# Kernel tuning notes

Hardware: AMD Instinct MI355X
Metric: run time of the kernel (lower is better)

The kernel has to match this reference:

```python
import jax, jax.numpy as jnp
import numpy as np

# dims per module source / chosen globals
B, LB = 4, 28            # new frames, buffered frames; M = B+LB = L = 32
DK, DV = 256, 32         # Dk=256 hardcoded; Dv = 4*len_of_lookup+4 with len_of_lookup=7
HS, WS = 64, 64          # H//8, W//8 with H=W=512
LMAX = 32                # memory cap L
TRAIN_SZ = 1000          # log base train_sz
ALPHA = 0.5              # blend coefficient (original inits 0, which zeroes the branch)
# log(L*h*w + h*w, train_sz) / sqrt(Dk)
SCALE = float(np.log(LMAX * HS * WS + HS * WS) / np.log(TRAIN_SZ) / np.sqrt(DK))


def _xavier(key, fan_in, fan_out):
    lim = np.sqrt(6.0 / (fan_in + fan_out))
    return jax.random.uniform(key, (fan_in, fan_out), jnp.float32, -lim, lim)


def setup_inputs() -> dict:
    key = jax.random.key(0)
    ks = jax.random.split(key, 7)
    return {
        "fc": jax.random.normal(ks[0], (B, DK, HS, WS), jnp.float32),
        "fm": jax.random.normal(ks[1], (B, DV, HS, WS), jnp.float32),
        "key_buffer": jax.random.normal(ks[2], (LB, DK, HS, WS), jnp.float32),
        "value_buffer": jax.random.normal(ks[3], (LB, DV, HS, WS), jnp.float32),
        "Q": _xavier(ks[4], DK, DK),
        "K": _xavier(ks[5], DK, DK),
        "V": _xavier(ks[6], DV, DV),
    }


def reference(fc, fm, key_buffer, value_buffer, Q, K, V):
    # matmul = einsum('ijkl,jm->imkl'): per-pixel channel mixing
    q = jnp.einsum('bdhw,de->behw', fc, Q)                      # [B,Dk,h,w]
    k = jnp.concatenate([jnp.einsum('bdhw,de->behw', fc, K), key_buffer], axis=0)    # [M,Dk,h,w]
    v = jnp.concatenate([jnp.einsum('bdhw,de->behw', fm, V), value_buffer], axis=0)  # [M,Dv,h,w]
    # current_batch (=1) < L, so no slicing of k/v on this step
    scores = SCALE * jnp.einsum('bdhw,mdhw->bmhw', q, k)        # [B,M,h,w]
    attn = jax.nn.softmax(scores, axis=-1)                      # NOTE: softmax over width axis, as in source (dim=-1)
    ctx = jnp.einsum('bmhw,mdhw->bdhw', attn, v)                # [B,Dv,h,w]
    return fm + ALPHA * ctx
```

## Files before the change

kernel.cpp:

```cpp
#include <hip/hip_runtime.h>
#include <hip/hip_bf16.h>
#include <cmath>

#define NB 4
#define NM 32
#define DKc 256
#define DVc 32
#define NP 4096

using bf16x8 = __attribute__((ext_vector_type(8))) short;
using f32x4  = __attribute__((ext_vector_type(4))) float;
using f32x2  = __attribute__((ext_vector_type(2))) float;

__device__ __forceinline__ unsigned short f2bf(float f) {
    union { float f; unsigned u; } x; x.f = f;
    unsigned r = 0x7FFFu + ((x.u >> 16) & 1u);
    return (unsigned short)((x.u + r) >> 16);
}

__global__ __launch_bounds__(256) void k_prep(
    const float* __restrict__ fc, unsigned short* __restrict__ fcT,
    const float* __restrict__ Q, unsigned short* __restrict__ WTq,
    const float* __restrict__ K, unsigned short* __restrict__ WTk,
    const float* __restrict__ fm, const float* __restrict__ V, float* __restrict__ vproj) {
    int x = blockIdx.x;
    int t = threadIdx.x;
    if (x < 1056) {
        __shared__ float tile[64][65];
        const float* s; unsigned short* d; int R, C, r0, c0;
        if (x < 1024) {
            int bb = x >> 8, rest = x & 255;
            R = 256; C = 4096;
            r0 = (rest >> 6) * 64; c0 = (rest & 63) * 64;
            s = fc + (long)bb * 256 * 4096; d = fcT + (long)bb * 256 * 4096;
        } else {
            int i = x - 1024;
            int mat = i >> 4, idx = i & 15;
            R = 256; C = 256;
            r0 = (idx >> 2) * 64; c0 = (idx & 3) * 64;
            s = mat ? K : Q; d = mat ? WTk : WTq;
        }
        #pragma unroll
        for (int j = 0; j < 16; ++j) {
            int i = t + 256 * j;
            int r = i >> 6, c = i & 63;
            tile[r][c] = s[(long)(r0 + r) * C + c0 + c];
        }
        __syncthreads();
        #pragma unroll
        for (int j = 0; j < 8; ++j) {
            int i = t + 256 * j;
            int row = i >> 5;
            int pr = i & 31;
            float f0 = tile[2 * pr][row];
            float f1 = tile[2 * pr + 1][row];
            unsigned pack = (unsigned)f2bf(f0) | ((unsigned)f2bf(f1) << 16);
            reinterpret_cast<unsigned*>(d)[(((long)(c0 + row) * R + r0) >> 1) + pr] = pack;
        }
    } else {
        __shared__ float Vl[32][32];
        __shared__ float fml[32][256];
        int i = x - 1056;
        int b = i >> 4, p0 = (i & 15) * 256;
        #pragma unroll
        for (int j = 0; j < 4; ++j) { int ii = t + 256 * j; Vl[ii >> 5][ii & 31] = V[ii]; }
        for (int j = 0; j < 32; ++j) {
            int ii = t + 256 * j;
            int dd = ii >> 8, c = ii & 255;
            fml[dd][c] = fm[((long)b * DVc + dd) * NP + p0 + c];
        }
        __syncthreads();
        float acc[32];
        #pragma unroll
        for (int e = 0; e < 32; ++e) acc[e] = 0.f;
        for (int dd = 0; dd < 32; ++dd) {
            float fv = fml[dd][t];
            #pragma unroll
            for (int e = 0; e < 32; ++e) acc[e] += fv * Vl[dd][e];
        }
        #pragma unroll
        for (int e = 0; e < 32; ++e) vproj[((long)b * DVc + e) * NP + p0 + t] = acc[e];
    }
}

__global__ __launch_bounds__(256) void k_proj(
    const unsigned short* __restrict__ WTq, const unsigned short* __restrict__ WTk,
    const unsigned short* __restrict__ fcT,
    float* __restrict__ qproj, float* __restrict__ kproj) {
    int t = threadIdx.x;
    int wave = t >> 6, lane = t & 63;
    int y = blockIdx.y;
    int b = y & 3, mat = y >> 2;
    int p0 = blockIdx.x * 32;
    int ln = lane & 15, quad = lane >> 4;
    const unsigned short* WT = mat ? WTk : WTq;
    float* dst = mat ? kproj : qproj;
    int e0w = wave * 64;
    const unsigned short* bbase = fcT + ((long)b * NP + p0 + ln) * DKc + quad * 8;
    f32x4 acc[4][2] = {};
    for (int kk = 0; kk < DKc; kk += 32) {
        bf16x8 a[4], bb[2];
        #pragma unroll
        for (int i = 0; i < 4; ++i)
            a[i] = *reinterpret_cast<const bf16x8*>(WT + (long)(e0w + i * 16 + ln) * DKc + quad * 8 + kk);
        #pragma unroll
        for (int j = 0; j < 2; ++j)
            bb[j] = *reinterpret_cast<const bf16x8*>(bbase + (long)j * 16 * DKc + kk);
        #pragma unroll
        for (int i = 0; i < 4; ++i)
            #pragma unroll
            for (int j = 0; j < 2; ++j)
                acc[i][j] = __builtin_amdgcn_mfma_f32_16x16x32_bf16(a[i], bb[j], acc[i][j], 0, 0, 0);
    }
    #pragma unroll
    for (int i = 0; i < 4; ++i)
        #pragma unroll
        for (int j = 0; j < 2; ++j)
            #pragma unroll
            for (int r = 0; r < 4; ++r) {
                int e = e0w + i * 16 + quad * 4 + r, p = p0 + j * 16 + ln;
                dst[((long)b * DKc + e) * NP + p] = acc[i][j][r];
            }
}

__global__ __launch_bounds__(1024) void k_fused(
    const float* __restrict__ qproj, const float* __restrict__ kproj,
    const float* __restrict__ kbuf, const float* __restrict__ vproj,
    const float* __restrict__ vbuf, const float* __restrict__ fm,
    float* __restrict__ out, float scale) {
    __shared__ float smem[16384];
    int t = threadIdx.x;
    int b = blockIdx.x >> 6, hrow = blockIdx.x & 63;
    int p0 = hrow * 64;
    int wave = t >> 6, lane = t & 63;
    int wg = lane & 15;

    {
        const float* qbase = qproj + (long)b * DKc * NP + p0;
        #pragma unroll
        for (int j = 0; j < 4; ++j) {
            int i = t + 1024 * j;
            int e = i >> 4, g = i & 15;
            *reinterpret_cast<f32x4*>(&smem[e * 64 + g * 4]) =
                *reinterpret_cast<const f32x4*>(qbase + (long)e * NP + g * 4);
        }
    }
    __syncthreads();

    {
        int mi = lane >> 4;
        int eh = wave >> 3, mq = wave & 7;
        int m = mq * 4 + mi;
        const float* kbase = (mq == 0 ? kproj + (long)m * DKc * NP
                                      : kbuf + (long)(m - 4) * DKc * NP)
                             + (long)(eh * 128) * NP + p0 + wg * 4;
        const float* qb = &smem[(eh * 128) * 64 + wg * 4];
        f32x4 s4 = {0.f, 0.f, 0.f, 0.f};
        for (int e8 = 0; e8 < 128; e8 += 8) {
            f32x4 kv[8], qv[8];
            #pragma unroll
            for (int u = 0; u < 8; ++u)
                kv[u] = *reinterpret_cast<const f32x4*>(kbase + (long)(e8 + u) * NP);
            #pragma unroll
            for (int u = 0; u < 8; ++u)
                qv[u] = *reinterpret_cast<const f32x4*>(qb + (e8 + u) * 64);
            #pragma unroll
            for (int u = 0; u < 8; ++u)
                s4 += qv[u] * kv[u];
        }
        __syncthreads();
        *reinterpret_cast<f32x4*>(&smem[eh * 2048 + m * 64 + wg * 4]) = s4;
    }
    __syncthreads();

    #pragma unroll
    for (int r = 0; r < 2; ++r) {
        int m = wave * 2 + r;
        float x = (smem[m * 64 + lane] + smem[2048 + m * 64 + lane]) * scale;
        float mx = x;
        #pragma unroll
        for (int dd = 1; dd < 64; dd <<= 1) mx = fmaxf(mx, __shfl_xor(mx, dd));
        float ev = __expf(x - mx);
        float sum = ev;
        #pragma unroll
        for (int dd = 1; dd < 64; dd <<= 1) sum += __shfl_xor(sum, dd);
        smem[4096 + m * 64 + lane] = ev / sum;
    }
    __syncthreads();

    {
        int di = lane >> 4;
        int mh = wave >> 3, dq = wave & 7;
        int dd = dq * 4 + di;
        f32x4 c4 = {0.f, 0.f, 0.f, 0.f};
        #pragma unroll
        for (int mm = 0; mm < 16; ++mm) {
            int m = mh * 16 + mm;
            const float* vb_ = (m < 4 ? vproj + (long)m * DVc * NP
                                      : vbuf + (long)(m - 4) * DVc * NP);
            f32x4 a4 = *reinterpret_cast<const f32x4*>(&smem[4096 + m * 64 + wg * 4]);
            f32x4 v4 = *reinterpret_cast<const f32x4*>(vb_ + (long)dd * NP + p0 + wg * 4);
            c4 += a4 * v4;
        }
        *reinterpret_cast<f32x4*>(&smem[mh * 2048 + dd * 64 + wg * 4]) = c4;
    }
    __syncthreads();

    #pragma unroll
    for (int r = 0; r < 2; ++r) {
        int i = t + 1024 * r;
        int dd = i >> 6, w = i & 63;
        float c = smem[dd * 64 + w] + smem[2048 + dd * 64 + w];
        long gi = ((long)b * DVc + dd) * NP + p0 + w;
        out[gi] = fm[gi] + 0.5f * c;
    }
}

extern "C" void kernel_launch(void* const* d_in, const int* in_sizes, int n_in,
                              void* d_out, int out_size, void* d_ws, size_t ws_size,
                              hipStream_t stream) {
    const float* fc = (const float*)d_in[0];
    const float* fm = (const float*)d_in[1];
    const float* kb = (const float*)d_in[2];
    const float* vb = (const float*)d_in[3];
    const float* Q  = (const float*)d_in[4];
    const float* K  = (const float*)d_in[5];
    const float* V  = (const float*)d_in[6];
    float* out = (float*)d_out;
    char* ws = (char*)d_ws;
    float*          qproj = (float*)(ws);
    float*          kproj = (float*)(ws + 16777216);
    float*          vproj = (float*)(ws + 33554432);
    unsigned short* fcT   = (unsigned short*)(ws + 35651584);
    unsigned short* WTq   = (unsigned short*)(ws + 44040192);
    unsigned short* WTk   = (unsigned short*)(ws + 44171264);
    float scale = (float)(log(135168.0) / log(1000.0) / 16.0);

    hipLaunchKernelGGL(k_prep, dim3(1120), dim3(256), 0, stream,
                       fc, fcT, Q, WTq, K, WTk, fm, V, vproj);
    hipLaunchKernelGGL(k_proj, dim3(128, 8), dim3(256), 0, stream,
                       WTq, WTk, fcT, qproj, kproj);
    hipLaunchKernelGGL(k_fused, dim3(256), dim3(1024), 0, stream,
                       qproj, kproj, kb, vproj, vb, fm, out, scale);
}
```

Baseline: 261.2 us.

## Restructure score computation with inline-asm double-buffered K loads and wider proj tiles

The scores phase of the fused kernel is rewritten. Each wave now owns a 16-channel slice of the key dimension for all 32 memory slots, keeps q in registers, and streams K rows through two 16-register buffers using inline-asm global_load_dword with explicit vmcnt waits. This overlaps the next slot's loads with the current FMAs and removes the LDS staging of q. Partial sums from the 16 waves are reduced through shared memory in two passes. Separately, the projection kernel doubles its pixel tile to 64 per block, which raises MFMA reuse of the weight fragments. The cost is more register pressure and fragile hand-written asm.

After: 252.4 us. -3.4%, faster.

```diff
diff --git a/kernel.cpp b/kernel.cpp
--- a/kernel.cpp
+++ b/kernel.cpp
@@ -91,37 +91,80 @@
     int wave = t >> 6, lane = t & 63;
     int y = blockIdx.y;
     int b = y & 3, mat = y >> 2;
-    int p0 = blockIdx.x * 32;
+    int p0 = blockIdx.x * 64;
     int ln = lane & 15, quad = lane >> 4;
     const unsigned short* WT = mat ? WTk : WTq;
     float* dst = mat ? kproj : qproj;
     int e0w = wave * 64;
     const unsigned short* bbase = fcT + ((long)b * NP + p0 + ln) * DKc + quad * 8;
-    f32x4 acc[4][2] = {};
+    f32x4 acc[4][4] = {};
     for (int kk = 0; kk < DKc; kk += 32) {
-        bf16x8 a[4], bb[2];
+        bf16x8 a[4], bb[4];
         #pragma unroll
         for (int i = 0; i < 4; ++i)
             a[i] = *reinterpret_cast<const bf16x8*>(WT + (long)(e0w + i * 16 + ln) * DKc + quad * 8 + kk);
         #pragma unroll
-        for (int j = 0; j < 2; ++j)
+        for (int j = 0; j < 4; ++j)
             bb[j] = *reinterpret_cast<const bf16x8*>(bbase + (long)j * 16 * DKc + kk);
         #pragma unroll
         for (int i = 0; i < 4; ++i)
             #pragma unroll
-            for (int j = 0; j < 2; ++j)
+            for (int j = 0; j < 4; ++j)
                 acc[i][j] = __builtin_amdgcn_mfma_f32_16x16x32_bf16(a[i], bb[j], acc[i][j], 0, 0, 0);
     }
     #pragma unroll
     for (int i = 0; i < 4; ++i)
         #pragma unroll
-        for (int j = 0; j < 2; ++j)
+        for (int j = 0; j < 4; ++j)
             #pragma unroll
             for (int r = 0; r < 4; ++r) {
                 int e = e0w + i * 16 + quad * 4 + r, p = p0 + j * 16 + ln;
                 dst[((long)b * DKc + e) * NP + p] = acc[i][j][r];
             }
 }
+
+#define LD16(K0, VO, BASE) do { unsigned _tv = (VO); asm volatile( \
+    "global_load_dword %0, %16, %17\n\t"  "v_add_u32 %16, 0x4000, %16\n\t" \
+    "global_load_dword %1, %16, %17\n\t"  "v_add_u32 %16, 0x4000, %16\n\t" \
+    "global_load_dword %2, %16, %17\n\t"  "v_add_u32 %16, 0x4000, %16\n\t" \
+    "global_load_dword %3, %16, %17\n\t"  "v_add_u32 %16, 0x4000, %16\n\t" \
+    "global_load_dword %4, %16, %17\n\t"  "v_add_u32 %16, 0x4000, %16\n\t" \
+    "global_load_dword %5, %16, %17\n\t"  "v_add_u32 %16, 0x4000, %16\n\t" \
+    "global_load_dword %6, %16, %17\n\t"  "v_add_u32 %16, 0x4000, %16\n\t" \
+    "global_load_dword %7, %16, %17\n\t"  "v_add_u32 %16, 0x4000, %16\n\t" \
+    "global_load_dword %8, %16, %17\n\t"  "v_add_u32 %16, 0x4000, %16\n\t" \
+    "global_load_dword %9, %16, %17\n\t"  "v_add_u32 %16, 0x4000, %16\n\t" \
+    "global_load_dword %10, %16, %17\n\t" "v_add_u32 %16, 0x4000, %16\n\t" \
+    "global_load_dword %11, %16, %17\n\t" "v_add_u32 %16, 0x4000, %16\n\t" \
+    "global_load_dword %12, %16, %17\n\t" "v_add_u32 %16, 0x4000, %16\n\t" \
+    "global_load_dword %13, %16, %17\n\t" "v_add_u32 %16, 0x4000, %16\n\t" \
+    "global_load_dword %14, %16, %17\n\t" "v_add_u32 %16, 0x4000, %16\n\t" \
+    "global_load_dword %15, %16, %17" \
+    : "=&v"(K0[0]), "=&v"(K0[1]), "=&v"(K0[2]), "=&v"(K0[3]), \
+      "=&v"(K0[4]), "=&v"(K0[5]), "=&v"(K0[6]), "=&v"(K0[7]), \
+      "=&v"(K0[8]), "=&v"(K0[9]), "=&v"(K0[10]), "=&v"(K0[11]), \
+      "=&v"(K0[12]), "=&v"(K0[13]), "=&v"(K0[14]), "=&v"(K0[15]), \
+      "+v"(_tv) \
+    : "s"(BASE) : "memory"); } while (0)
+
+#define KWAIT16 do { asm volatile("s_waitcnt vmcnt(16)" ::: "memory"); \
+                     __builtin_amdgcn_sched_barrier(0); } while (0)
+#define KWAIT0  do { asm volatile("s_waitcnt vmcnt(0)"  ::: "memory"); \
+                     __builtin_amdgcn_sched_barrier(0); } while (0)
+
+#define FMA16(M, KV) do { \
+    acc[M] = fmaf(qr[0],  KV[0],  acc[M]); acc[M] = fmaf(qr[1],  KV[1],  acc[M]); \
+    acc[M] = fmaf(qr[2],  KV[2],  acc[M]); acc[M] = fmaf(qr[3],  KV[3],  acc[M]); \
+    acc[M] = fmaf(qr[4],  KV[4],  acc[M]); acc[M] = fmaf(qr[5],  KV[5],  acc[M]); \
+    acc[M] = fmaf(qr[6],  KV[6],  acc[M]); acc[M] = fmaf(qr[7],  KV[7],  acc[M]); \
+    acc[M] = fmaf(qr[8],  KV[8],  acc[M]); acc[M] = fmaf(qr[9],  KV[9],  acc[M]); \
+    acc[M] = fmaf(qr[10], KV[10], acc[M]); acc[M] = fmaf(qr[11], KV[11], acc[M]); \
+    acc[M] = fmaf(qr[12], KV[12], acc[M]); acc[M] = fmaf(qr[13], KV[13], acc[M]); \
+    acc[M] = fmaf(qr[14], KV[14], acc[M]); acc[M] = fmaf(qr[15], KV[15], acc[M]); \
+  } while (0)
+
+#define KBASE(M) ((M) < 4 ? kproj + (size_t)(M) * KMS : kbuf + (size_t)((M) - 4) * KMS)
+#define STG(M, KV) KWAIT16; FMA16(M, KV); LD16(KV, vo, KBASE((M) + 2));
 
 __global__ __launch_bounds__(1024) void k_fused(
     const float* __restrict__ qproj, const float* __restrict__ kproj,
@@ -135,57 +178,56 @@
     int wave = t >> 6, lane = t & 63;
     int wg = lane & 15;
 
-    {
-        const float* qbase = qproj + (long)b * DKc * NP + p0;
-        #pragma unroll
-        for (int j = 0; j < 4; ++j) {
-            int i = t + 1024 * j;
-            int e = i >> 4, g = i & 15;
-            *reinterpret_cast<f32x4*>(&smem[e * 64 + g * 4]) =
-                *reinterpret_cast<const f32x4*>(qbase + (long)e * NP + g * 4);
-        }
-    }
-    __syncthreads();
-
-    {
-        int mi = lane >> 4;
-        int eh = wave >> 3, mq = wave & 7;
-        int m = mq * 4 + mi;
-        const float* kbase = (mq == 0 ? kproj + (long)m * DKc * NP
-                                      : kbuf + (long)(m - 4) * DKc * NP)
-                             + (long)(eh * 128) * NP + p0 + wg * 4;
-        const float* qb = &smem[(eh * 128) * 64 + wg * 4];
-        f32x4 s4 = {0.f, 0.f, 0.f, 0.f};
-        for (int e8 = 0; e8 < 128; e8 += 8) {
-            f32x4 kv[8], qv[8];
-            #pragma unroll
-            for (int u = 0; u < 8; ++u)
-                kv[u] = *reinterpret_cast<const f32x4*>(kbase + (long)(e8 + u) * NP);
-            #pragma unroll
-            for (int u = 0; u < 8; ++u)
-                qv[u] = *reinterpret_cast<const f32x4*>(qb + (e8 + u) * 64);
-            #pragma unroll
-            for (int u = 0; u < 8; ++u)
-                s4 += qv[u] * kv[u];
-        }
-        __syncthreads();
-        *reinterpret_cast<f32x4*>(&smem[eh * 2048 + m * 64 + wg * 4]) = s4;
-    }
-    __syncthreads();
-
+    const size_t KMS = (size_t)DKc * NP;
+    float qr[16], kA[16], kB[16], acc[32];
+    #pragma unroll
+    for (int m = 0; m < 32; ++m) acc[m] = 0.f;
+
+    unsigned vo = (unsigned)((wave * 16 * NP + p0 + lane) * 4);
+    const float* qb = qproj + (size_t)b * KMS;
+
+    LD16(qr, vo, qb);
+    LD16(kA, vo, KBASE(0));
+    LD16(kB, vo, KBASE(1));
+    STG(0, kA)  STG(1, kB)  STG(2, kA)  STG(3, kB)  STG(4, kA)  STG(5, kB)
+    STG(6, kA)  STG(7, kB)  STG(8, kA)  STG(9, kB)  STG(10, kA) STG(11, kB)
+    STG(12, kA) STG(13, kB) STG(14, kA) STG(15, kB) STG(16, kA) STG(17, kB)
+    STG(18, kA) STG(19, kB) STG(20, kA) STG(21, kB) STG(22, kA) STG(23, kB)
+    STG(24, kA) STG(25, kB) STG(26, kA) STG(27, kB) STG(28, kA) STG(29, kB)
+    KWAIT16; FMA16(30, kA);
+    KWAIT0;  FMA16(31, kB);
+
+    if (wave < 8) {
+        #pragma unroll
+        for (int m = 0; m < 32; ++m) smem[wave * 2048 + m * 64 + lane] = acc[m];
+    }
+    __syncthreads();
+    if (wave >= 8) {
+        #pragma unroll
+        for (int m = 0; m < 32; ++m) smem[(wave - 8) * 2048 + m * 64 + lane] += acc[m];
+    }
+    __syncthreads();
+
+    float att[2];
     #pragma unroll
     for (int r = 0; r < 2; ++r) {
         int m = wave * 2 + r;
-        float x = (smem[m * 64 + lane] + smem[2048 + m * 64 + lane]) * scale;
+        float x = 0.f;
+        #pragma unroll
+        for (int s = 0; s < 8; ++s) x += smem[s * 2048 + m * 64 + lane];
+        x *= scale;
         float mx = x;
         #pragma unroll
-        for (int dd = 1; dd < 64; dd <<= 1) mx = fmaxf(mx, __shfl_xor(mx, dd));
+        for (int d = 1; d < 64; d <<= 1) mx = fmaxf(mx, __shfl_xor(mx, d));
         float ev = __expf(x - mx);
         float sum = ev;
         #pragma unroll
-        for (int dd = 1; dd < 64; dd <<= 1) sum += __shfl_xor(sum, dd);
-        smem[4096 + m * 64 + lane] = ev / sum;
-    }
+        for (int d = 1; d < 64; d <<= 1) sum += __shfl_xor(sum, d);
+        att[r] = ev / sum;
+    }
+    __syncthreads();
+    smem[(wave * 2) * 64 + lane] = att[0];
+    smem[(wave * 2 + 1) * 64 + lane] = att[1];
     __syncthreads();
 
     {
@@ -198,20 +240,20 @@
             int m = mh * 16 + mm;
             const float* vb_ = (m < 4 ? vproj + (long)m * DVc * NP
                                       : vbuf + (long)(m - 4) * DVc * NP);
-            f32x4 a4 = *reinterpret_cast<const f32x4*>(&smem[4096 + m * 64 + wg * 4]);
+            f32x4 a4 = *reinterpret_cast<const f32x4*>(&smem[m * 64 + wg * 4]);
             f32x4 v4 = *reinterpret_cast<const f32x4*>(vb_ + (long)dd * NP + p0 + wg * 4);
             c4 += a4 * v4;
         }
-        *reinterpret_cast<f32x4*>(&smem[mh * 2048 + dd * 64 + wg * 4]) = c4;
+        *reinterpret_cast<f32x4*>(&smem[4096 + mh * 2048 + dd * 64 + wg * 4]) = c4;
     }
     __syncthreads();
 
     #pragma unroll
     for (int r = 0; r < 2; ++r) {
         int i = t + 1024 * r;
-        int dd = i >> 6, w = i & 63;
-        float c = smem[dd * 64 + w] + smem[2048 + dd * 64 + w];
-        long gi = ((long)b * DVc + dd) * NP + p0 + w;
+        int dd2 = i >> 6, w2 = i & 63;
+        float c = smem[4096 + dd2 * 64 + w2] + smem[4096 + 2048 + dd2 * 64 + w2];
+        long gi = ((long)b * DVc + dd2) * NP + p0 + w2;
         out[gi] = fm[gi] + 0.5f * c;
     }
 }
@@ -238,7 +280,7 @@
 
     hipLaunchKernelGGL(k_prep, dim3(1120), dim3(256), 0, stream,
                        fc, fcT, Q, WTq, K, WTk, fm, V, vproj);
-    hipLaunchKernelGGL(k_proj, dim3(128, 8), dim3(256), 0, stream,
+    hipLaunchKernelGGL(k_proj, dim3(64, 8), dim3(256), 0, stream,
                        WTq, WTk, fcT, qproj, kproj);
     hipLaunchKernelGGL(k_fused, dim3(256), dim3(1024), 0, stream,
                        qproj, kproj, kb, vproj, vb, fm, out, scale);
```

## Software-pipeline fused score loads with inline asm triple buffering and direct q reads

Applied to the files above, without the earlier changes.

The score stage of the fused kernel now reads q straight from global memory instead of staging it in shared memory. It streams k and q rows through three register slots using hand-written global_load_dwordx4 asm with explicit vmcnt waits, so loads stay in flight while FMAs run. Base pointers are made wave-uniform with readfirstlane so the loads can use scalar base plus 32-bit vector offsets. Shared memory shrinks and a minimum-blocks launch bound is added. The projection kernel tile also doubles to 64 pixels per block. Risks: the asm bypasses compiler scheduling, and the stricter launch bound may cap registers and cause spills.

Result: no change. 262.9 us (+0.6%).

```diff
diff --git a/kernel.cpp b/kernel.cpp
--- a/kernel.cpp
+++ b/kernel.cpp
@@ -16,6 +16,13 @@
     union { float f; unsigned u; } x; x.f = f;
     unsigned r = 0x7FFFu + ((x.u >> 16) & 1u);
     return (unsigned short)((x.u + r) >> 16);
+}
+
+__device__ __forceinline__ const float* rfl_ptr(const float* p) {
+    unsigned long long u = (unsigned long long)p;
+    unsigned lo = __builtin_amdgcn_readfirstlane((unsigned)u);
+    unsigned hi = __builtin_amdgcn_readfirstlane((unsigned)(u >> 32));
+    return (const float*)(((unsigned long long)hi << 32) | lo);
 }
 
 __global__ __launch_bounds__(256) void k_prep(
@@ -91,31 +98,31 @@
     int wave = t >> 6, lane = t & 63;
     int y = blockIdx.y;
     int b = y & 3, mat = y >> 2;
-    int p0 = blockIdx.x * 32;
+    int p0 = blockIdx.x * 64;
     int ln = lane & 15, quad = lane >> 4;
     const unsigned short* WT = mat ? WTk : WTq;
     float* dst = mat ? kproj : qproj;
     int e0w = wave * 64;
     const unsigned short* bbase = fcT + ((long)b * NP + p0 + ln) * DKc + quad * 8;
-    f32x4 acc[4][2] = {};
+    f32x4 acc[4][4] = {};
     for (int kk = 0; kk < DKc; kk += 32) {
-        bf16x8 a[4], bb[2];
+        bf16x8 a[4], bb[4];
         #pragma unroll
         for (int i = 0; i < 4; ++i)
             a[i] = *reinterpret_cast<const bf16x8*>(WT + (long)(e0w + i * 16 + ln) * DKc + quad * 8 + kk);
         #pragma unroll
-        for (int j = 0; j < 2; ++j)
+        for (int j = 0; j < 4; ++j)
             bb[j] = *reinterpret_cast<const bf16x8*>(bbase + (long)j * 16 * DKc + kk);
         #pragma unroll
         for (int i = 0; i < 4; ++i)
             #pragma unroll
-            for (int j = 0; j < 2; ++j)
+            for (int j = 0; j < 4; ++j)
                 acc[i][j] = __builtin_amdgcn_mfma_f32_16x16x32_bf16(a[i], bb[j], acc[i][j], 0, 0, 0);
     }
     #pragma unroll
     for (int i = 0; i < 4; ++i)
         #pragma unroll
-        for (int j = 0; j < 2; ++j)
+        for (int j = 0; j < 4; ++j)
             #pragma unroll
             for (int r = 0; r < 4; ++r) {
                 int e = e0w + i * 16 + quad * 4 + r, p = p0 + j * 16 + ln;
@@ -123,69 +130,93 @@
             }
 }
 
-__global__ __launch_bounds__(1024) void k_fused(
+#define LD8_I(K0,K1,K2,K3,Q0,Q1,Q2,Q3) asm volatile( \
+    "global_load_dwordx4 %0, %8, %10\n\t"  "v_add_u32 %8, 0x4000, %8\n\t" \
+    "global_load_dwordx4 %1, %8, %10\n\t"  "v_add_u32 %8, 0x4000, %8\n\t" \
+    "global_load_dwordx4 %2, %8, %10\n\t"  "v_add_u32 %8, 0x4000, %8\n\t" \
+    "global_load_dwordx4 %3, %8, %10\n\t"  "v_add_u32 %8, 0x4000, %8\n\t" \
+    "global_load_dwordx4 %4, %9, %11\n\t"  "v_add_u32 %9, 0x4000, %9\n\t" \
+    "global_load_dwordx4 %5, %9, %11\n\t"  "v_add_u32 %9, 0x4000, %9\n\t" \
+    "global_load_dwordx4 %6, %9, %11\n\t"  "v_add_u32 %9, 0x4000, %9\n\t" \
+    "global_load_dwordx4 %7, %9, %11" \
+    : "=&v"(K0), "=&v"(K1), "=&v"(K2), "=&v"(K3), \
+      "=&v"(Q0), "=&v"(Q1), "=&v"(Q2), "=&v"(Q3), "+v"(vk), "+v"(vq) \
+    : "s"(kb_s), "s"(qb_s) : "memory"); \
+    asm volatile("v_add_u32 %0, 0x4000, %0" : "+v"(vq));
+#define LD8(...) LD8_I(__VA_ARGS__)
+
+#define W16 do { asm volatile("s_waitcnt vmcnt(16)" ::: "memory"); \
+                 __builtin_amdgcn_sched_barrier(0); } while (0)
+#define W8  do { asm volatile("s_waitcnt vmcnt(8)"  ::: "memory"); \
+                 __builtin_amdgcn_sched_barrier(0); } while (0)
+#define W0  do { asm volatile("s_waitcnt vmcnt(0)"  ::: "memory"); \
+                 __builtin_amdgcn_sched_barrier(0); } while (0)
+
+#define FMAS_I(K0,K1,K2,K3,Q0,Q1,Q2,Q3) { c4 += Q0*K0; c4 += Q1*K1; c4 += Q2*K2; c4 += Q3*K3; }
+#define FMAS(...) FMAS_I(__VA_ARGS__)
+
+#define SLOT_A ka0,ka1,ka2,ka3,qa0,qa1,qa2,qa3
+#define SLOT_B kb0,kb1,kb2,kb3,qb0,qb1,qb2,qb3
+#define SLOT_C kc0,kc1,kc2,kc3,qc0,qc1,qc2,qc3
+#define STEP(SL) W16; FMAS(SL); LD8(SL);
+
+__global__ __launch_bounds__(1024, 4) void k_fused(
     const float* __restrict__ qproj, const float* __restrict__ kproj,
     const float* __restrict__ kbuf, const float* __restrict__ vproj,
     const float* __restrict__ vbuf, const float* __restrict__ fm,
     float* __restrict__ out, float scale) {
-    __shared__ float smem[16384];
+    __shared__ float smem[6144];
     int t = threadIdx.x;
     int b = blockIdx.x >> 6, hrow = blockIdx.x & 63;
     int p0 = hrow * 64;
     int wave = t >> 6, lane = t & 63;
-    int wg = lane & 15;
+    int wg = lane & 15, mi = lane >> 4;
+    const size_t KMS = (size_t)DKc * NP;
 
     {
-        const float* qbase = qproj + (long)b * DKc * NP + p0;
-        #pragma unroll
-        for (int j = 0; j < 4; ++j) {
-            int i = t + 1024 * j;
-            int e = i >> 4, g = i & 15;
-            *reinterpret_cast<f32x4*>(&smem[e * 64 + g * 4]) =
-                *reinterpret_cast<const f32x4*>(qbase + (long)e * NP + g * 4);
-        }
-    }
-    __syncthreads();
-
-    {
-        int mi = lane >> 4;
-        int eh = wave >> 3, mq = wave & 7;
-        int m = mq * 4 + mi;
-        const float* kbase = (mq == 0 ? kproj + (long)m * DKc * NP
-                                      : kbuf + (long)(m - 4) * DKc * NP)
-                             + (long)(eh * 128) * NP + p0 + wg * 4;
-        const float* qb = &smem[(eh * 128) * 64 + wg * 4];
-        f32x4 s4 = {0.f, 0.f, 0.f, 0.f};
-        for (int e8 = 0; e8 < 128; e8 += 8) {
-            f32x4 kv[8], qv[8];
-            #pragma unroll
-            for (int u = 0; u < 8; ++u)
-                kv[u] = *reinterpret_cast<const f32x4*>(kbase + (long)(e8 + u) * NP);
-            #pragma unroll
-            for (int u = 0; u < 8; ++u)
-                qv[u] = *reinterpret_cast<const f32x4*>(qb + (e8 + u) * 64);
-            #pragma unroll
-            for (int u = 0; u < 8; ++u)
-                s4 += qv[u] * kv[u];
-        }
-        __syncthreads();
-        *reinterpret_cast<f32x4*>(&smem[eh * 2048 + m * 64 + wg * 4]) = s4;
-    }
-    __syncthreads();
-
+        int eh = wave >> 3, mg = wave & 7;
+        const float* kb_s = rfl_ptr((mg == 0 ? kproj : kbuf + (size_t)(mg * 4 - 4) * KMS)
+                                    + (size_t)eh * 128 * NP);
+        const float* qb_s = rfl_ptr(qproj + (size_t)b * KMS + (size_t)eh * 128 * NP);
+        unsigned vk = (unsigned)(((size_t)mi * KMS + p0 + wg * 4) * 4);
+        unsigned vq = (unsigned)((p0 + wg * 4) * 4);
+
+        f32x4 ka0,ka1,ka2,ka3,qa0,qa1,qa2,qa3;
+        f32x4 kb0,kb1,kb2,kb3,qb0,qb1,qb2,qb3;
+        f32x4 kc0,kc1,kc2,kc3,qc0,qc1,qc2,qc3;
+        f32x4 c4 = {0.f, 0.f, 0.f, 0.f};
+
+        LD8(SLOT_A) LD8(SLOT_B) LD8(SLOT_C)
+        STEP(SLOT_A) STEP(SLOT_B) STEP(SLOT_C) STEP(SLOT_A) STEP(SLOT_B) STEP(SLOT_C)
+        STEP(SLOT_A) STEP(SLOT_B) STEP(SLOT_C) STEP(SLOT_A) STEP(SLOT_B) STEP(SLOT_C)
+        STEP(SLOT_A) STEP(SLOT_B) STEP(SLOT_C) STEP(SLOT_A) STEP(SLOT_B) STEP(SLOT_C)
+        STEP(SLOT_A) STEP(SLOT_B) STEP(SLOT_C) STEP(SLOT_A) STEP(SLOT_B) STEP(SLOT_C)
+        STEP(SLOT_A) STEP(SLOT_B) STEP(SLOT_C) STEP(SLOT_A) STEP(SLOT_B)
+        W16; FMAS(SLOT_C);
+        W8;  FMAS(SLOT_A);
+        W0;  FMAS(SLOT_B);
+        int m = mg * 4 + mi;
+        *reinterpret_cast<f32x4*>(&smem[eh * 2048 + m * 64 + wg * 4]) = c4;
+    }
+    __syncthreads();
+
+    float att0, att1;
     #pragma unroll
     for (int r = 0; r < 2; ++r) {
         int m = wave * 2 + r;
         float x = (smem[m * 64 + lane] + smem[2048 + m * 64 + lane]) * scale;
         float mx = x;
         #pragma unroll
-        for (int dd = 1; dd < 64; dd <<= 1) mx = fmaxf(mx, __shfl_xor(mx, dd));
+        for (int d = 1; d < 64; d <<= 1) mx = fmaxf(mx, __shfl_xor(mx, d));
         float ev = __expf(x - mx);
         float sum = ev;
         #pragma unroll
-        for (int dd = 1; dd < 64; dd <<= 1) sum += __shfl_xor(sum, dd);
-        smem[4096 + m * 64 + lane] = ev / sum;
-    }
+        for (int d = 1; d < 64; d <<= 1) sum += __shfl_xor(sum, d);
+        if (r == 0) att0 = ev / sum; else att1 = ev / sum;
+    }
+    __syncthreads();
+    smem[(wave * 2) * 64 + lane] = att0;
+    smem[(wave * 2 + 1) * 64 + lane] = att1;
     __syncthreads();
 
     {
@@ -198,20 +229,20 @@
             int m = mh * 16 + mm;
             const float* vb_ = (m < 4 ? vproj + (long)m * DVc * NP
                                       : vbuf + (long)(m - 4) * DVc * NP);
-            f32x4 a4 = *reinterpret_cast<const f32x4*>(&smem[4096 + m * 64 + wg * 4]);
+            f32x4 a4 = *reinterpret_cast<const f32x4*>(&smem[m * 64 + wg * 4]);
             f32x4 v4 = *reinterpret_cast<const f32x4*>(vb_ + (long)dd * NP + p0 + wg * 4);
             c4 += a4 * v4;
         }
-        *reinterpret_cast<f32x4*>(&smem[mh * 2048 + dd * 64 + wg * 4]) = c4;
+        *reinterpret_cast<f32x4*>(&smem[2048 + mh * 2048 + dd * 64 + wg * 4]) = c4;
     }
     __syncthreads();
 
     #pragma unroll
     for (int r = 0; r < 2; ++r) {
         int i = t + 1024 * r;
-        int dd = i >> 6, w = i & 63;
-        float c = smem[dd * 64 + w] + smem[2048 + dd * 64 + w];
-        long gi = ((long)b * DVc + dd) * NP + p0 + w;
+        int dd2 = i >> 6, w2 = i & 63;
+        float c = smem[2048 + dd2 * 64 + w2] + smem[4096 + dd2 * 64 + w2];
+        long gi = ((long)b * DVc + dd2) * NP + p0 + w2;
         out[gi] = fm[gi] + 0.5f * c;
     }
 }
@@ -238,7 +269,7 @@
 
     hipLaunchKernelGGL(k_prep, dim3(1120), dim3(256), 0, stream,
                        fc, fcT, Q, WTq, K, WTk, fm, V, vproj);
-    hipLaunchKernelGGL(k_proj, dim3(128, 8), dim3(256), 0, stream,
+    hipLaunchKernelGGL(k_proj, dim3(64, 8), dim3(256), 0, stream,
                        WTq, WTk, fcT, qproj, kproj);
     hipLaunchKernelGGL(k_fused, dim3(256), dim3(1024), 0, stream,
                        qproj, kproj, kb, vproj, vb, fm, out, scale);
```
